# Kernel tuning notes

Measured on AMD Instinct MI355X. Metric: run time of the kernel, lower is better.

Reference implementation:

```python
import jax, jax.numpy as jnp
import numpy as np

N, E, L, F, HID, OUT = 20000, 200000, 5, 4, 128, 3


def _lin(x, w, b):
    # torch Linear convention: w is [out, in]
    return x @ w.T + b


def setup_inputs() -> dict:
    key = jax.random.key(0)
    ks = iter(jax.random.split(key, 40))
    nrm = lambda shape, s=0.05: jax.random.normal(next(ks), shape, dtype=jnp.float32) * s
    inp = {
        'x': jax.random.normal(next(ks), (N, L, F), dtype=jnp.float32),
        'edge_index': jax.random.randint(next(ks), (2, E), 0, N, dtype=jnp.int64),
        'edge_attr': jax.random.normal(next(ks), (E, F), dtype=jnp.float32),
        'batch': jnp.zeros((N,), dtype=jnp.int64),
        'node_type': jax.random.normal(next(ks), (N, 1), dtype=jnp.float32),
        # PastStateEncoder params
        'emb': nrm((L, F), 1.0),
        'conv_w': nrm((HID, 2 * F, 3)),  # Conv1d(8,128,3) OIW
        'conv_b': nrm((HID,)),
        # FusionLayer Linear(129,128)
        'fuse_w': nrm((HID, HID + 1)), 'fuse_b': nrm((HID,)),
        # gnn1 EdgeModel: Linear(2*128+4,128), Linear(128,128)
        'g1e_w1': nrm((HID, 2 * HID + F)), 'g1e_b1': nrm((HID,)),
        'g1e_w2': nrm((HID, HID)), 'g1e_b2': nrm((HID,)),
        # gnn1 NodeModel: Linear(256,128), Linear(128,128)
        'g1n_w1': nrm((HID, 2 * HID)), 'g1n_b1': nrm((HID,)),
        'g1n_w2': nrm((HID, HID)), 'g1n_b2': nrm((HID,)),
        # gnn2 EdgeModel: Linear(2*128+128,128), Linear(128,128)
        'g2e_w1': nrm((HID, 3 * HID)), 'g2e_b1': nrm((HID,)),
        'g2e_w2': nrm((HID, HID)), 'g2e_b2': nrm((HID,)),
        # gnn2 NodeModel
        'g2n_w1': nrm((HID, 2 * HID)), 'g2n_b1': nrm((HID,)),
        'g2n_w2': nrm((HID, HID)), 'g2n_b2': nrm((HID,)),
        # final_mlp: Linear(128,128), BN(128), Linear(128,3)
        'fm_w1': nrm((HID, HID)), 'fm_b1': nrm((HID,)),
        'bn_g': jnp.ones((HID,), dtype=jnp.float32), 'bn_b': jnp.zeros((HID,), dtype=jnp.float32),
        'fm_w2': nrm((OUT, HID)), 'fm_b2': nrm((OUT,)),
    }
    return inp


def _encoder(x, emb, conv_w, conv_b):
    # x: [N, L, F]; append learned positional embedding -> [N, L, 2F]
    n = x.shape[0]
    xe = jnp.concatenate([x, jnp.broadcast_to(emb[None], (n, L, F))], axis=-1)
    xc = xe.transpose(0, 2, 1)  # [N, 2F, L]
    y = jax.lax.conv_general_dilated(
        xc, conv_w, window_strides=(1,), padding=[(1, 1)],
        dimension_numbers=('NCW', 'OIW', 'NCW'))
    y = y + conv_b[None, :, None]
    return y.mean(axis=-1)  # [N, HID]


def _edge_mlp(src, dst, ea, w1, b1, w2, b2):
    h = jax.nn.relu(_lin(jnp.concatenate([src, dst, ea], axis=1), w1, b1))
    return _lin(h, w2, b2)


def _node_mlp(x_row, ea, w1, b1, w2, b2):
    h = jax.nn.relu(_lin(jnp.concatenate([x_row, ea], axis=1), w1, b1))
    return _lin(h, w2, b2)


def reference(x, edge_index, edge_attr, batch, node_type,
              emb, conv_w, conv_b, fuse_w, fuse_b,
              g1e_w1, g1e_b1, g1e_w2, g1e_b2, g1n_w1, g1n_b1, g1n_w2, g1n_b2,
              g2e_w1, g2e_b1, g2e_w2, g2e_b2, g2n_w1, g2n_b1, g2n_w2, g2n_b2,
              fm_w1, fm_b1, bn_g, bn_b, fm_w2, fm_b2):
    row, col = edge_index[0], edge_index[1]
    h = _encoder(x, emb, conv_w, conv_b)                     # [N,128]
    h = _lin(jnp.concatenate([h, node_type], axis=-1), fuse_w, fuse_b)  # [N,128]
    # gnn1 (MetaLayer: edge model then node model; node model here is per-edge)
    ea = _edge_mlp(h[row], h[col], edge_attr, g1e_w1, g1e_b1, g1e_w2, g1e_b2)  # [E,128]
    h = _node_mlp(h[row], ea, g1n_w1, g1n_b1, g1n_w2, g1n_b2)                  # [E,128]
    # gnn2 (h now lives on edges; indices < N <= E remain valid, matching torch)
    ea = _edge_mlp(h[row], h[col], ea, g2e_w1, g2e_b1, g2e_w2, g2e_b2)
    h = _node_mlp(h[row], ea, g2n_w1, g2n_b1, g2n_w2, g2n_b2)
    # final head on edge_attr: Linear -> BatchNorm1d (training stats) -> ReLU -> Linear
    z = _lin(ea, fm_w1, fm_b1)
    mu = z.mean(axis=0)
    var = z.var(axis=0)  # biased, matches torch BN normalization
    z = (z - mu) * jax.lax.rsqrt(var + 1e-5) * bn_g + bn_b
    z = jax.nn.relu(z)
    return _lin(z, fm_w2, fm_b2)  # [E,3]
```

## Files before the change

kernel.cpp:

```cpp
#include <hip/hip_runtime.h>

#define N_NODES 20000
#define N_EDGES 200000
#define HID 128
#define STR 136
#define NBLK 3125

typedef unsigned short u16;
using bf16x8 = __attribute__((ext_vector_type(8))) __bf16;
using f32x4  = __attribute__((ext_vector_type(4))) float;

__device__ __forceinline__ u16 f2bf(float f) {
  union { float f; unsigned u; } v; v.f = f;
  unsigned u = v.u;
  return (u16)((u + 0x7FFFu + ((u >> 16) & 1u)) >> 16);
}
__device__ __forceinline__ float bf2f(unsigned s) {
  union { unsigned u; float f; } v; v.u = s << 16;
  return v.f;
}
__device__ __forceinline__ bf16x8 ld8(const u16* p) { return *(const bf16x8*)p; }

__device__ __forceinline__ void zero_acc(f32x4 acc[4][2]) {
#pragma unroll
  for (int i = 0; i < 4; ++i) {
    acc[i][0] = (f32x4){0.f, 0.f, 0.f, 0.f};
    acc[i][1] = (f32x4){0.f, 0.f, 0.f, 0.f};
  }
}

template <int KSTEPS, typename AF>
__device__ __forceinline__ void wgemm(const u16* __restrict__ PW, AF afrag,
                                      f32x4 acc[4][2], int lane, int wave) {
  const u16* pb = PW + (wave * 2 * 64 + lane) * 8;
  bf16x8 b0[2], b1[2];
  b0[0] = ld8(pb);
  b1[0] = ld8(pb + 512);
#pragma unroll
  for (int ks = 0; ks < KSTEPS; ++ks) {
    const int cur = ks & 1, nxt = cur ^ 1;
    if (ks + 1 < KSTEPS) {
      b0[nxt] = ld8(pb + (ks + 1) * 4096);
      b1[nxt] = ld8(pb + (ks + 1) * 4096 + 512);
    }
#pragma unroll
    for (int mt = 0; mt < 4; ++mt) {
      bf16x8 a = afrag(ks, mt);
      acc[mt][0] = __builtin_amdgcn_mfma_f32_16x16x32_bf16(a, b0[cur], acc[mt][0], 0, 0, 0);
      acc[mt][1] = __builtin_amdgcn_mfma_f32_16x16x32_bf16(a, b1[cur], acc[mt][1], 0, 0, 0);
    }
  }
}

template <bool RELU>
__device__ __forceinline__ void epi_store(u16* buf, const f32x4 acc[4][2],
                                          const float* __restrict__ bias,
                                          int lane, int wave) {
  const int c = lane & 15, q = lane >> 4;
  const float bb0 = bias[wave * 32 + c], bb1 = bias[wave * 32 + 16 + c];
#pragma unroll
  for (int mt = 0; mt < 4; ++mt)
#pragma unroll
    for (int nt = 0; nt < 2; ++nt) {
      const float bb = nt ? bb1 : bb0;
      const int col = wave * 32 + nt * 16 + c;
#pragma unroll
      for (int r = 0; r < 4; ++r) {
        float v = acc[mt][nt][r] + bb;
        if (RELU) v = fmaxf(v, 0.f);
        buf[(mt * 16 + q * 4 + r) * STR + col] = f2bf(v);
      }
    }
}

__device__ __forceinline__ void flush_buf(const u16* buf, u16* __restrict__ gout,
                                          int e0, int tid) {
#pragma unroll
  for (int it = 0; it < 4; ++it) {
    int cid = tid + it * 256, e = cid >> 4, p = cid & 15;
    uint4 v = *(const uint4*)(buf + e * STR + p * 8);
    *(uint4*)(gout + (size_t)(e0 + e) * HID + p * 8) = v;
  }
}

__device__ __forceinline__ void stage_gather(const int* __restrict__ rowI,
                                             const int* __restrict__ colI,
                                             const u16* __restrict__ htab,
                                             u16* B0, u16* B1,
                                             int e0, int lane, int wave) {
  const int r = lane >> 4, p = lane & 15;
#pragma unroll
  for (int it = 0; it < 8; ++it) {
    int j = wave * 32 + it * 4 + r;
    int e = j & 63;
    int id = (j < 64) ? rowI[e0 + e] : colI[e0 + e];
    uint4 v = *(const uint4*)(htab + (size_t)id * HID + p * 8);
    *(uint4*)(((j < 64) ? B0 : B1) + e * STR + p * 8) = v;
  }
}

__global__ void k_fold(const float* __restrict__ emb, const float* __restrict__ conv_w,
                       const float* __restrict__ conv_b, const float* __restrict__ fuse_w,
                       const float* __restrict__ fuse_b,
                       const float* __restrict__ fm_w1, const float* __restrict__ g2e_b2,
                       const float* __restrict__ fm_b1,
                       float* __restrict__ Mt, float* __restrict__ C0,
                       float* __restrict__ Wnt, float* __restrict__ b67) {
  __shared__ float Ash[128][21];
  int o = threadIdx.x;
  {
    float b0 = conv_b[o];
#pragma unroll
    for (int p = 0; p < 5; ++p) {
#pragma unroll
      for (int i = 0; i < 8; ++i) {
        float s = 0.f;
#pragma unroll
        for (int k = 0; k < 3; ++k) {
          int t = p + 1 - k;
          if (t >= 0 && t < 5) s += conv_w[(o * 8 + i) * 3 + k];
        }
        s *= 0.2f;
        if (i < 4) Ash[o][p * 4 + i] = s;
        else b0 += emb[p * 4 + (i - 4)] * s;
      }
    }
    Ash[o][20] = b0;
  }
  __syncthreads();
  float m[20];
#pragma unroll
  for (int qq = 0; qq < 20; ++qq) m[qq] = 0.f;
  float c0 = fuse_b[o];
  for (int j = 0; j < 128; ++j) {
    float w = fuse_w[o * 129 + j];
#pragma unroll
    for (int qq = 0; qq < 20; ++qq) m[qq] += w * Ash[j][qq];
    c0 += w * Ash[j][20];
  }
#pragma unroll
  for (int qq = 0; qq < 20; ++qq) Mt[qq * 128 + o] = m[qq];
  C0[o] = c0;
  Wnt[o] = fuse_w[o * 129 + 128];
  float sb = 0.f;
  for (int j = 0; j < 128; ++j) sb += fm_w1[o * 128 + j] * g2e_b2[j];
  b67[o] = sb + fm_b1[o];
}

__global__ void k_fold2(const float* __restrict__ w6, const float* __restrict__ w7,
                        float* __restrict__ W67) {
  int o = blockIdx.x;
  int k = threadIdx.x;
  float s = 0.f;
  for (int j = 0; j < 128; ++j) s += w7[o * 128 + j] * w6[j * 128 + k];
  W67[o * 128 + k] = s;
}

struct PackArgs {
  const float* src[6];
  u16* dst[6];
  int Kin[6];
  int ksCum[7];
};

__global__ void k_pack(PackArgs pa) {
  int bk = blockIdx.x;
  int mi = 0;
  while (bk >= pa.ksCum[mi + 1]) ++mi;
  int ks = bk - pa.ksCum[mi];
  const float* W = pa.src[mi];
  u16* D = pa.dst[mi] + ks * 4096;
  int Kin = pa.Kin[mi];
#pragma unroll
  for (int t = 0; t < 16; ++t) {
    int el = t * 256 + (int)threadIdx.x;
    int j = el & 7, ln = (el >> 3) & 63, ntile = el >> 9;
    int k = ks * 32 + ((ln >> 4) << 3) + j;
    int n = ntile * 16 + (ln & 15);
    float v = (k < Kin) ? W[n * Kin + k] : 0.0f;
    D[el] = f2bf(v);
  }
}

__global__ __launch_bounds__(256) void k_encode(const float* __restrict__ x,
                                                const float* __restrict__ node_type,
                                                const float* __restrict__ Mt,
                                                const float* __restrict__ C0,
                                                const float* __restrict__ Wnt,
                                                u16* __restrict__ h2) {
  __shared__ float xs[16][20], nts[16], mts[20 * 128];
  const int tid = threadIdx.x;
  const int n0 = blockIdx.x * 16;
  for (int i = tid; i < 320; i += 256) xs[i / 20][i % 20] = x[n0 * 20 + i];
  if (tid < 16) nts[tid] = node_type[n0 + tid];
  for (int i = tid; i < 2560; i += 256) mts[i] = Mt[i];
  __syncthreads();
  const int nl = tid >> 4;
  const int c0 = (tid & 15) * 8;
  float nt = nts[nl];
  union { u16 s[8]; uint4 u; } o;
#pragma unroll
  for (int i = 0; i < 8; ++i) {
    int ch = c0 + i;
    float acc = C0[ch] + Wnt[ch] * nt;
#pragma unroll
    for (int qq = 0; qq < 20; ++qq) acc += xs[nl][qq] * mts[qq * 128 + ch];
    o.s[i] = f2bf(acc);
  }
  *(uint4*)(h2 + (size_t)(n0 + nl) * HID + c0) = o.u;
}

__global__ __launch_bounds__(256, 4) void k_gnn1(
    const int* __restrict__ eidx, const float* __restrict__ eattr,
    const u16* __restrict__ h2, const u16* __restrict__ pW1, const u16* __restrict__ pW2,
    const u16* __restrict__ pW3, const u16* __restrict__ pW4, const float* __restrict__ b1,
    const float* __restrict__ b2, const float* __restrict__ b3, const float* __restrict__ b4,
    u16* __restrict__ ea1, u16* __restrict__ h3) {
  __shared__ __align__(16) u16 B0[64 * STR], B1[64 * STR];
  const int tid = threadIdx.x, lane = tid & 63, wave = tid >> 6;
  const int e0 = blockIdx.x * 64;
  const int m = lane & 15, q = lane >> 4;
  const int aoff = m * STR + q * 8;
  const int* rowI = eidx;
  const int* colI = eidx + N_EDGES;

  stage_gather(rowI, colI, h2, B0, B1, e0, lane, wave);

  bf16x8 ef[4];
#pragma unroll
  for (int mt = 0; mt < 4; ++mt) {
    union { u16 s[8]; uint4 u; bf16x8 v; } t;
    t.u = make_uint4(0u, 0u, 0u, 0u);
    if (q == 0) {
      float4 a = *(const float4*)(eattr + (size_t)(e0 + mt * 16 + m) * 4);
      t.s[0] = f2bf(a.x); t.s[1] = f2bf(a.y); t.s[2] = f2bf(a.z); t.s[3] = f2bf(a.w);
    }
    ef[mt] = t.v;
  }
  __syncthreads();

  f32x4 acc[4][2];
  zero_acc(acc);
  wgemm<9>(pW1, [&](int ks, int mt) -> bf16x8 {
    if (ks < 4) return ld8(B0 + aoff + mt * 16 * STR + ks * 32);
    if (ks < 8) return ld8(B1 + aoff + mt * 16 * STR + (ks - 4) * 32);
    return ef[mt];
  }, acc, lane, wave);
  __syncthreads();
  epi_store<true>(B1, acc, b1, lane, wave);
  __syncthreads();

  zero_acc(acc);
  wgemm<4>(pW2, [&](int ks, int mt) -> bf16x8 {
    return ld8(B1 + aoff + mt * 16 * STR + ks * 32);
  }, acc, lane, wave);
  epi_store<false>(B0, acc, b2, lane, wave);
  __syncthreads();
  flush_buf(B0, ea1, e0, tid);

  if (e0 < N_NODES) {
#pragma unroll
    for (int it = 0; it < 4; ++it) {
      int e = wave * 16 + it * 4 + q;
      int id = rowI[e0 + e];
      uint4 v = *(const uint4*)(h2 + (size_t)id * HID + m * 8);
      *(uint4*)(B1 + e * STR + m * 8) = v;
    }
    __syncthreads();

    zero_acc(acc);
    wgemm<8>(pW3, [&](int ks, int mt) -> bf16x8 {
      if (ks < 4) return ld8(B1 + aoff + mt * 16 * STR + ks * 32);
      return ld8(B0 + aoff + mt * 16 * STR + (ks - 4) * 32);
    }, acc, lane, wave);
    __syncthreads();
    epi_store<true>(B1, acc, b3, lane, wave);
    __syncthreads();

    zero_acc(acc);
    wgemm<4>(pW4, [&](int ks, int mt) -> bf16x8 {
      return ld8(B1 + aoff + mt * 16 * STR + ks * 32);
    }, acc, lane, wave);
    epi_store<false>(B0, acc, b4, lane, wave);
    __syncthreads();
    flush_buf(B0, h3, e0, tid);
  }
}

__global__ __launch_bounds__(256, 4) void k_gnn2(
    const int* __restrict__ eidx, const u16* __restrict__ h3, u16* ea1z,
    const u16* __restrict__ pW5, const u16* __restrict__ pW67,
    const float* __restrict__ b5, const float* __restrict__ b67,
    float* __restrict__ partials) {
  __shared__ __align__(16) u16 B0[64 * STR], B1[64 * STR];
  const int tid = threadIdx.x, lane = tid & 63, wave = tid >> 6;
  const int e0 = blockIdx.x * 64;
  const int m = lane & 15, q = lane >> 4;
  const int aoff = m * STR + q * 8;
  const int* rowI = eidx;
  const int* colI = eidx + N_EDGES;

  stage_gather(rowI, colI, h3, B0, B1, e0, lane, wave);
  __syncthreads();

  f32x4 acc[4][2];
  zero_acc(acc);
  wgemm<8>(pW5, [&](int ks, int mt) -> bf16x8 {
    if (ks < 4) return ld8(B0 + aoff + mt * 16 * STR + ks * 32);
    return ld8(B1 + aoff + mt * 16 * STR + (ks - 4) * 32);
  }, acc, lane, wave);
  __syncthreads();

#pragma unroll
  for (int it = 0; it < 4; ++it) {
    int cid = tid + it * 256, e = cid >> 4, p = cid & 15;
    uint4 v = *(const uint4*)(ea1z + (size_t)(e0 + e) * HID + p * 8);
    *(uint4*)(B0 + e * STR + p * 8) = v;
  }
  __syncthreads();

  wgemm<4>(pW5 + 8 * 4096, [&](int ks, int mt) -> bf16x8 {
    return ld8(B0 + aoff + mt * 16 * STR + ks * 32);
  }, acc, lane, wave);
  epi_store<true>(B1, acc, b5, lane, wave);
  __syncthreads();

  zero_acc(acc);
  wgemm<4>(pW67, [&](int ks, int mt) -> bf16x8 {
    return ld8(B1 + aoff + mt * 16 * STR + ks * 32);
  }, acc, lane, wave);

  {
    const int c = lane & 15;
    const float bb0 = b67[wave * 32 + c], bb1 = b67[wave * 32 + 16 + c];
    float s0 = 0.f, q0 = 0.f, s1 = 0.f, q1 = 0.f;
#pragma unroll
    for (int mt = 0; mt < 4; ++mt)
#pragma unroll
      for (int r = 0; r < 4; ++r) {
        float v0 = acc[mt][0][r] + bb0;
        float v1 = acc[mt][1][r] + bb1;
        s0 += v0; q0 += v0 * v0;
        s1 += v1; q1 += v1 * v1;
        int row = mt * 16 + q * 4 + r;
        B0[row * STR + wave * 32 + c] = f2bf(v0);
        B0[row * STR + wave * 32 + 16 + c] = f2bf(v1);
      }
    s0 += __shfl_xor(s0, 16); s0 += __shfl_xor(s0, 32);
    q0 += __shfl_xor(q0, 16); q0 += __shfl_xor(q0, 32);
    s1 += __shfl_xor(s1, 16); s1 += __shfl_xor(s1, 32);
    q1 += __shfl_xor(q1, 16); q1 += __shfl_xor(q1, 32);
    if (lane < 16) {
      int base = (int)blockIdx.x * 256;
      partials[base + wave * 32 + lane] = s0;
      partials[base + wave * 32 + 16 + lane] = s1;
      partials[base + 128 + wave * 32 + lane] = q0;
      partials[base + 128 + wave * 32 + 16 + lane] = q1;
    }
  }
  __syncthreads();
  flush_buf(B0, ea1z, e0, tid);
}

__global__ void k_reduce(const float* __restrict__ partials, float* __restrict__ bnacc,
                         int nrows) {
  int t = threadIdx.x;
  float s = 0.f;
  for (int b = blockIdx.x; b < nrows; b += 64) s += partials[b * 256 + t];
  atomicAdd(&bnacc[t], s);
}

__global__ __launch_bounds__(256) void k_head(const u16* __restrict__ z,
                                              const float* __restrict__ bnacc,
                                              const float* __restrict__ bn_g,
                                              const float* __restrict__ bn_b,
                                              const float* __restrict__ w2,
                                              const float* __restrict__ b2,
                                              float* __restrict__ out) {
  __shared__ float sh_s[128], sh_h[128], sh_w0[128], sh_w1[128], sh_w2[128];
  const int tid = threadIdx.x;
  if (tid < 128) {
    const float inv = 1.0f / (float)N_EDGES;
    float mu = bnacc[tid] * inv;
    float var = bnacc[128 + tid] * inv - mu * mu;
    float sc = bn_g[tid] * rsqrtf(var + 1e-5f);
    sh_s[tid] = sc;
    sh_h[tid] = bn_b[tid] - mu * sc;
    sh_w0[tid] = w2[tid];
    sh_w1[tid] = w2[128 + tid];
    sh_w2[tid] = w2[256 + tid];
  }
  __syncthreads();
  const int e = blockIdx.x * 256 + tid;
  if (e >= N_EDGES) return;
  float a0 = b2[0], a1 = b2[1], a2 = b2[2];
  const u16* zr = z + (size_t)e * HID;
#pragma unroll
  for (int p = 0; p < 16; ++p) {
    uint4 v = *(const uint4*)(zr + p * 8);
    unsigned wv[4] = {v.x, v.y, v.z, v.w};
#pragma unroll
    for (int k = 0; k < 4; ++k) {
      int ch = p * 8 + k * 2;
      float lo = bf2f(wv[k] & 0xffffu), hi = bf2f(wv[k] >> 16);
      float r0 = fmaxf(fmaf(lo, sh_s[ch], sh_h[ch]), 0.f);
      float r1 = fmaxf(fmaf(hi, sh_s[ch + 1], sh_h[ch + 1]), 0.f);
      a0 += r0 * sh_w0[ch] + r1 * sh_w0[ch + 1];
      a1 += r0 * sh_w1[ch] + r1 * sh_w1[ch + 1];
      a2 += r0 * sh_w2[ch] + r1 * sh_w2[ch + 1];
    }
  }
  out[e * 3 + 0] = a0;
  out[e * 3 + 1] = a1;
  out[e * 3 + 2] = a2;
}

extern "C" void kernel_launch(void* const* d_in, const int* in_sizes, int n_in,
                              void* d_out, int out_size, void* d_ws, size_t ws_size,
                              hipStream_t stream) {
  const float* x         = (const float*)d_in[0];
  const int* eidx        = (const int*)d_in[1];
  const float* eattr     = (const float*)d_in[2];
  const float* node_type = (const float*)d_in[4];
  const float* emb       = (const float*)d_in[5];
  const float* conv_w    = (const float*)d_in[6];
  const float* conv_b    = (const float*)d_in[7];
  const float* fuse_w    = (const float*)d_in[8];
  const float* fuse_b    = (const float*)d_in[9];
  const float* g1e_w1    = (const float*)d_in[10];
  const float* g1e_b1    = (const float*)d_in[11];
  const float* g1e_w2    = (const float*)d_in[12];
  const float* g1e_b2    = (const float*)d_in[13];
  const float* g1n_w1    = (const float*)d_in[14];
  const float* g1n_b1    = (const float*)d_in[15];
  const float* g1n_w2    = (const float*)d_in[16];
  const float* g1n_b2    = (const float*)d_in[17];
  const float* g2e_w1    = (const float*)d_in[18];
  const float* g2e_b1    = (const float*)d_in[19];
  const float* g2e_w2    = (const float*)d_in[20];
  const float* g2e_b2    = (const float*)d_in[21];
  const float* fm_w1     = (const float*)d_in[26];
  const float* fm_b1     = (const float*)d_in[27];
  const float* bn_g      = (const float*)d_in[28];
  const float* bn_b      = (const float*)d_in[29];
  const float* fm_w2     = (const float*)d_in[30];
  const float* fm_b2     = (const float*)d_in[31];
  float* out = (float*)d_out;

  char* ws = (char*)d_ws;
  size_t off = 0;
  auto take = [&](size_t bytes) {
    void* p = ws + off;
    off = (off + bytes + 255) & ~(size_t)255;
    return p;
  };
  u16* h2   = (u16*)take((size_t)N_NODES * HID * 2);
  u16* h3   = (u16*)take((size_t)20032 * HID * 2);
  u16* ea1z = (u16*)take((size_t)N_EDGES * HID * 2);
  float* Mt    = (float*)take(20 * 128 * 4);
  float* C0    = (float*)take(128 * 4);
  float* Wnt   = (float*)take(128 * 4);
  float* bnacc = (float*)take(256 * 4);
  float* b67   = (float*)take(128 * 4);
  float* W67f  = (float*)take(128 * 128 * 4);
  float* partials = (float*)take((size_t)NBLK * 256 * 4);
  u16* pW1  = (u16*)take(9 * 4096 * 2);
  u16* pW2  = (u16*)take(4 * 4096 * 2);
  u16* pW3  = (u16*)take(8 * 4096 * 2);
  u16* pW4  = (u16*)take(4 * 4096 * 2);
  u16* pW5  = (u16*)take(12 * 4096 * 2);
  u16* pW67 = (u16*)take(4 * 4096 * 2);

  hipMemsetAsync(bnacc, 0, 256 * 4, stream);
  k_fold<<<1, 128, 0, stream>>>(emb, conv_w, conv_b, fuse_w, fuse_b,
                                fm_w1, g2e_b2, fm_b1, Mt, C0, Wnt, b67);
  k_fold2<<<128, 128, 0, stream>>>(g2e_w2, fm_w1, W67f);

  PackArgs pa;
  const float* srcs[6] = {g1e_w1, g1e_w2, g1n_w1, g1n_w2, g2e_w1, W67f};
  u16* dsts[6] = {pW1, pW2, pW3, pW4, pW5, pW67};
  int kins[6] = {260, 128, 256, 128, 384, 128};
  int kst[6] = {9, 4, 8, 4, 12, 4};
  int cum = 0;
  for (int i = 0; i < 6; ++i) {
    pa.src[i] = srcs[i]; pa.dst[i] = dsts[i]; pa.Kin[i] = kins[i];
    pa.ksCum[i] = cum; cum += kst[i];
  }
  pa.ksCum[6] = cum;
  k_pack<<<41, 256, 0, stream>>>(pa);

  k_encode<<<N_NODES / 16, 256, 0, stream>>>(x, node_type, Mt, C0, Wnt, h2);
  k_gnn1<<<NBLK, 256, 0, stream>>>(eidx, eattr, h2, pW1, pW2, pW3, pW4,
                                   g1e_b1, g1e_b2, g1n_b1, g1n_b2, ea1z, h3);
  k_gnn2<<<NBLK, 256, 0, stream>>>(eidx, h3, ea1z, pW5, pW67,
                                   g2e_b1, b67, partials);
  k_reduce<<<64, 256, 0, stream>>>(partials, bnacc, NBLK);
  k_head<<<(N_EDGES + 255) / 256, 256, 0, stream>>>(ea1z, bnacc, bn_g, bn_b,
                                                    fm_w2, fm_b2, out);
}
```

Before: 277.3 us.

## Merge prep kernels, use replicated atomic BN stats, and coalesce head reads

Folds k_fold and k_fold2 into one 128-block prep kernel that parallelises the weight folding across blocks, and merges weight packing with node encoding into a single launch. The per-block BN partials buffer and the k_reduce kernel are replaced by atomics into 64 replicated slots, which k_head sums itself. k_head now has each group of 16 lanes read one edge row contiguously and reduce with shuffles, so global loads coalesce. This cuts launch count and memory traffic, at the cost of atomic contention and nondeterministic float summation order.

Measured after the change: 237.5 us. 1.17x faster.

```diff
diff --git a/kernel.cpp b/kernel.cpp
--- a/kernel.cpp
+++ b/kernel.cpp
@@ -5,6 +5,7 @@
 #define HID 128
 #define STR 136
 #define NBLK 3125
+#define NREP 64
 
 typedef unsigned short u16;
 using bf16x8 = __attribute__((ext_vector_type(8))) __bf16;
@@ -99,17 +100,21 @@
   }
 }
 
-__global__ void k_fold(const float* __restrict__ emb, const float* __restrict__ conv_w,
-                       const float* __restrict__ conv_b, const float* __restrict__ fuse_w,
-                       const float* __restrict__ fuse_b,
-                       const float* __restrict__ fm_w1, const float* __restrict__ g2e_b2,
-                       const float* __restrict__ fm_b1,
-                       float* __restrict__ Mt, float* __restrict__ C0,
-                       float* __restrict__ Wnt, float* __restrict__ b67) {
-  __shared__ float Ash[128][21];
-  int o = threadIdx.x;
+__global__ __launch_bounds__(128) void k_prep1(
+    const float* __restrict__ emb, const float* __restrict__ conv_w,
+    const float* __restrict__ conv_b, const float* __restrict__ fuse_w,
+    const float* __restrict__ fuse_b,
+    const float* __restrict__ fm_w1, const float* __restrict__ g2e_b2,
+    const float* __restrict__ fm_b1, const float* __restrict__ w6,
+    float* __restrict__ Mt, float* __restrict__ C0, float* __restrict__ Wnt,
+    float* __restrict__ b67, float* __restrict__ W67) {
+  __shared__ float red[22][129];
+  __shared__ float w7s[128];
+  const int o = blockIdx.x;
+  const int j = threadIdx.x;
+  float A[21];
   {
-    float b0 = conv_b[o];
+    float b0 = conv_b[j];
 #pragma unroll
     for (int p = 0; p < 5; ++p) {
 #pragma unroll
@@ -118,42 +123,33 @@
 #pragma unroll
         for (int k = 0; k < 3; ++k) {
           int t = p + 1 - k;
-          if (t >= 0 && t < 5) s += conv_w[(o * 8 + i) * 3 + k];
+          if (t >= 0 && t < 5) s += conv_w[(j * 8 + i) * 3 + k];
         }
         s *= 0.2f;
-        if (i < 4) Ash[o][p * 4 + i] = s;
+        if (i < 4) A[p * 4 + i] = s;
         else b0 += emb[p * 4 + (i - 4)] * s;
       }
     }
-    Ash[o][20] = b0;
-  }
-  __syncthreads();
-  float m[20];
-#pragma unroll
-  for (int qq = 0; qq < 20; ++qq) m[qq] = 0.f;
-  float c0 = fuse_b[o];
-  for (int j = 0; j < 128; ++j) {
-    float w = fuse_w[o * 129 + j];
-#pragma unroll
-    for (int qq = 0; qq < 20; ++qq) m[qq] += w * Ash[j][qq];
-    c0 += w * Ash[j][20];
-  }
-#pragma unroll
-  for (int qq = 0; qq < 20; ++qq) Mt[qq * 128 + o] = m[qq];
-  C0[o] = c0;
-  Wnt[o] = fuse_w[o * 129 + 128];
-  float sb = 0.f;
-  for (int j = 0; j < 128; ++j) sb += fm_w1[o * 128 + j] * g2e_b2[j];
-  b67[o] = sb + fm_b1[o];
-}
-
-__global__ void k_fold2(const float* __restrict__ w6, const float* __restrict__ w7,
-                        float* __restrict__ W67) {
-  int o = blockIdx.x;
-  int k = threadIdx.x;
+    A[20] = b0;
+  }
+  float w = fuse_w[o * 129 + j];
+  float w7 = fm_w1[o * 128 + j];
+  w7s[j] = w7;
+#pragma unroll
+  for (int qq = 0; qq < 21; ++qq) red[qq][j] = w * A[qq];
+  red[21][j] = w7 * g2e_b2[j];
+  __syncthreads();
+  if (j < 22) {
+    float s = 0.f;
+    for (int t = 0; t < 128; ++t) s += red[j][t];
+    if (j < 20)      Mt[j * 128 + o] = s;
+    else if (j == 20) C0[o] = s + fuse_b[o];
+    else              b67[o] = s + fm_b1[o];
+  }
+  if (j == 0) Wnt[o] = fuse_w[o * 129 + 128];
   float s = 0.f;
-  for (int j = 0; j < 128; ++j) s += w7[o * 128 + j] * w6[j * 128 + k];
-  W67[o * 128 + k] = s;
+  for (int t = 0; t < 128; ++t) s += w7s[t] * w6[t * 128 + j];
+  W67[o * 128 + j] = s;
 }
 
 struct PackArgs {
@@ -163,34 +159,32 @@
   int ksCum[7];
 };
 
-__global__ void k_pack(PackArgs pa) {
-  int bk = blockIdx.x;
-  int mi = 0;
-  while (bk >= pa.ksCum[mi + 1]) ++mi;
-  int ks = bk - pa.ksCum[mi];
-  const float* W = pa.src[mi];
-  u16* D = pa.dst[mi] + ks * 4096;
-  int Kin = pa.Kin[mi];
-#pragma unroll
-  for (int t = 0; t < 16; ++t) {
-    int el = t * 256 + (int)threadIdx.x;
-    int j = el & 7, ln = (el >> 3) & 63, ntile = el >> 9;
-    int k = ks * 32 + ((ln >> 4) << 3) + j;
-    int n = ntile * 16 + (ln & 15);
-    float v = (k < Kin) ? W[n * Kin + k] : 0.0f;
-    D[el] = f2bf(v);
-  }
-}
-
-__global__ __launch_bounds__(256) void k_encode(const float* __restrict__ x,
-                                                const float* __restrict__ node_type,
-                                                const float* __restrict__ Mt,
-                                                const float* __restrict__ C0,
-                                                const float* __restrict__ Wnt,
-                                                u16* __restrict__ h2) {
+__global__ __launch_bounds__(256) void k_prep2(
+    PackArgs pa, const float* __restrict__ x, const float* __restrict__ node_type,
+    const float* __restrict__ Mt, const float* __restrict__ C0,
+    const float* __restrict__ Wnt, u16* __restrict__ h2) {
+  if (blockIdx.x < 41) {
+    int bk = blockIdx.x;
+    int mi = 0;
+    while (bk >= pa.ksCum[mi + 1]) ++mi;
+    int ks = bk - pa.ksCum[mi];
+    const float* W = pa.src[mi];
+    u16* D = pa.dst[mi] + ks * 4096;
+    int Kin = pa.Kin[mi];
+#pragma unroll
+    for (int t = 0; t < 16; ++t) {
+      int el = t * 256 + (int)threadIdx.x;
+      int j = el & 7, ln = (el >> 3) & 63, ntile = el >> 9;
+      int k = ks * 32 + ((ln >> 4) << 3) + j;
+      int n = ntile * 16 + (ln & 15);
+      float v = (k < Kin) ? W[n * Kin + k] : 0.0f;
+      D[el] = f2bf(v);
+    }
+    return;
+  }
   __shared__ float xs[16][20], nts[16], mts[20 * 128];
   const int tid = threadIdx.x;
-  const int n0 = blockIdx.x * 16;
+  const int n0 = ((int)blockIdx.x - 41) * 16;
   for (int i = tid; i < 320; i += 256) xs[i / 20][i % 20] = x[n0 * 20 + i];
   if (tid < 16) nts[tid] = node_type[n0 + tid];
   for (int i = tid; i < 2560; i += 256) mts[i] = Mt[i];
@@ -291,7 +285,7 @@
     const int* __restrict__ eidx, const u16* __restrict__ h3, u16* ea1z,
     const u16* __restrict__ pW5, const u16* __restrict__ pW67,
     const float* __restrict__ b5, const float* __restrict__ b67,
-    float* __restrict__ partials) {
+    float* __restrict__ bnrep) {
   __shared__ __align__(16) u16 B0[64 * STR], B1[64 * STR];
   const int tid = threadIdx.x, lane = tid & 63, wave = tid >> 6;
   const int e0 = blockIdx.x * 64;
@@ -351,27 +345,19 @@
     s1 += __shfl_xor(s1, 16); s1 += __shfl_xor(s1, 32);
     q1 += __shfl_xor(q1, 16); q1 += __shfl_xor(q1, 32);
     if (lane < 16) {
-      int base = (int)blockIdx.x * 256;
-      partials[base + wave * 32 + lane] = s0;
-      partials[base + wave * 32 + 16 + lane] = s1;
-      partials[base + 128 + wave * 32 + lane] = q0;
-      partials[base + 128 + wave * 32 + 16 + lane] = q1;
+      float* slot = bnrep + ((int)blockIdx.x & (NREP - 1)) * 256;
+      atomicAdd(&slot[wave * 32 + lane], s0);
+      atomicAdd(&slot[wave * 32 + 16 + lane], s1);
+      atomicAdd(&slot[128 + wave * 32 + lane], q0);
+      atomicAdd(&slot[128 + wave * 32 + 16 + lane], q1);
     }
   }
   __syncthreads();
   flush_buf(B0, ea1z, e0, tid);
 }
 
-__global__ void k_reduce(const float* __restrict__ partials, float* __restrict__ bnacc,
-                         int nrows) {
-  int t = threadIdx.x;
-  float s = 0.f;
-  for (int b = blockIdx.x; b < nrows; b += 64) s += partials[b * 256 + t];
-  atomicAdd(&bnacc[t], s);
-}
-
 __global__ __launch_bounds__(256) void k_head(const u16* __restrict__ z,
-                                              const float* __restrict__ bnacc,
+                                              const float* __restrict__ bnrep,
                                               const float* __restrict__ bn_g,
                                               const float* __restrict__ bn_b,
                                               const float* __restrict__ w2,
@@ -379,29 +365,40 @@
                                               float* __restrict__ out) {
   __shared__ float sh_s[128], sh_h[128], sh_w0[128], sh_w1[128], sh_w2[128];
   const int tid = threadIdx.x;
-  if (tid < 128) {
-    const float inv = 1.0f / (float)N_EDGES;
-    float mu = bnacc[tid] * inv;
-    float var = bnacc[128 + tid] * inv - mu * mu;
-    float sc = bn_g[tid] * rsqrtf(var + 1e-5f);
-    sh_s[tid] = sc;
-    sh_h[tid] = bn_b[tid] - mu * sc;
-    sh_w0[tid] = w2[tid];
-    sh_w1[tid] = w2[128 + tid];
-    sh_w2[tid] = w2[256 + tid];
-  }
-  __syncthreads();
-  const int e = blockIdx.x * 256 + tid;
-  if (e >= N_EDGES) return;
-  float a0 = b2[0], a1 = b2[1], a2 = b2[2];
-  const u16* zr = z + (size_t)e * HID;
-#pragma unroll
-  for (int p = 0; p < 16; ++p) {
-    uint4 v = *(const uint4*)(zr + p * 8);
+  {
+    float s = 0.f;
+    for (int r = 0; r < NREP; ++r) s += bnrep[r * 256 + tid];
+    __shared__ float acc2[256];
+    acc2[tid] = s;
+    __syncthreads();
+    if (tid < 128) {
+      const float inv = 1.0f / (float)N_EDGES;
+      float mu = acc2[tid] * inv;
+      float var = acc2[128 + tid] * inv - mu * mu;
+      float sc = bn_g[tid] * rsqrtf(var + 1e-5f);
+      sh_s[tid] = sc;
+      sh_h[tid] = bn_b[tid] - mu * sc;
+      sh_w0[tid] = w2[tid];
+      sh_w1[tid] = w2[128 + tid];
+      sh_w2[tid] = w2[256 + tid];
+    }
+    __syncthreads();
+  }
+  const int lane = tid & 63, wave = tid >> 6;
+  const int g = lane >> 4;
+  const int p = lane & 15;
+  const int c0 = p * 8;
+  const float bb0 = b2[0], bb1 = b2[1], bb2 = b2[2];
+#pragma unroll 4
+  for (int it = 0; it < 16; ++it) {
+    int e = (int)blockIdx.x * 256 + wave * 64 + it * 4 + g;
+    if (e >= N_EDGES) break;
+    uint4 v = *(const uint4*)(z + (size_t)e * HID + c0);
     unsigned wv[4] = {v.x, v.y, v.z, v.w};
+    float a0 = 0.f, a1 = 0.f, a2 = 0.f;
 #pragma unroll
     for (int k = 0; k < 4; ++k) {
-      int ch = p * 8 + k * 2;
+      int ch = c0 + k * 2;
       float lo = bf2f(wv[k] & 0xffffu), hi = bf2f(wv[k] >> 16);
       float r0 = fmaxf(fmaf(lo, sh_s[ch], sh_h[ch]), 0.f);
       float r1 = fmaxf(fmaf(hi, sh_s[ch + 1], sh_h[ch + 1]), 0.f);
@@ -409,10 +406,14 @@
       a1 += r0 * sh_w1[ch] + r1 * sh_w1[ch + 1];
       a2 += r0 * sh_w2[ch] + r1 * sh_w2[ch + 1];
     }
-  }
-  out[e * 3 + 0] = a0;
-  out[e * 3 + 1] = a1;
-  out[e * 3 + 2] = a2;
+#pragma unroll
+    for (int off = 1; off < 16; off <<= 1) {
+      a0 += __shfl_xor(a0, off);
+      a1 += __shfl_xor(a1, off);
+      a2 += __shfl_xor(a2, off);
+    }
+    if (p < 3) out[e * 3 + p] = (p == 0) ? a0 + bb0 : (p == 1) ? a1 + bb1 : a2 + bb2;
+  }
 }
 
 extern "C" void kernel_launch(void* const* d_in, const int* in_sizes, int n_in,
@@ -460,10 +461,9 @@
   float* Mt    = (float*)take(20 * 128 * 4);
   float* C0    = (float*)take(128 * 4);
   float* Wnt   = (float*)take(128 * 4);
-  float* bnacc = (float*)take(256 * 4);
   float* b67   = (float*)take(128 * 4);
   float* W67f  = (float*)take(128 * 128 * 4);
-  float* partials = (float*)take((size_t)NBLK * 256 * 4);
+  float* bnrep = (float*)take((size_t)NREP * 256 * 4);
   u16* pW1  = (u16*)take(9 * 4096 * 2);
   u16* pW2  = (u16*)take(4 * 4096 * 2);
   u16* pW3  = (u16*)take(8 * 4096 * 2);
@@ -471,10 +471,10 @@
   u16* pW5  = (u16*)take(12 * 4096 * 2);
   u16* pW67 = (u16*)take(4 * 4096 * 2);
 
-  hipMemsetAsync(bnacc, 0, 256 * 4, stream);
-  k_fold<<<1, 128, 0, stream>>>(emb, conv_w, conv_b, fuse_w, fuse_b,
-                                fm_w1, g2e_b2, fm_b1, Mt, C0, Wnt, b67);
-  k_fold2<<<128, 128, 0, stream>>>(g2e_w2, fm_w1, W67f);
+  hipMemsetAsync(bnrep, 0, (size_t)NREP * 256 * 4, stream);
+  k_prep1<<<128, 128, 0, stream>>>(emb, conv_w, conv_b, fuse_w, fuse_b,
+                                   fm_w1, g2e_b2, fm_b1, g2e_w2,
+                                   Mt, C0, Wnt, b67, W67f);
 
   PackArgs pa;
   const float* srcs[6] = {g1e_w1, g1e_w2, g1n_w1, g1n_w2, g2e_w1, W67f};
@@ -487,14 +487,12 @@
     pa.ksCum[i] = cum; cum += kst[i];
   }
   pa.ksCum[6] = cum;
-  k_pack<<<41, 256, 0, stream>>>(pa);
-
-  k_encode<<<N_NODES / 16, 256, 0, stream>>>(x, node_type, Mt, C0, Wnt, h2);
+
+  k_prep2<<<41 + N_NODES / 16, 256, 0, stream>>>(pa, x, node_type, Mt, C0, Wnt, h2);
   k_gnn1<<<NBLK, 256, 0, stream>>>(eidx, eattr, h2, pW1, pW2, pW3, pW4,
                                    g1e_b1, g1e_b2, g1n_b1, g1n_b2, ea1z, h3);
   k_gnn2<<<NBLK, 256, 0, stream>>>(eidx, h3, ea1z, pW5, pW67,
-                                   g2e_b1, b67, partials);
-  k_reduce<<<64, 256, 0, stream>>>(partials, bnacc, NBLK);
-  k_head<<<(N_EDGES + 255) / 256, 256, 0, stream>>>(ea1z, bnacc, bn_g, bn_b,
+                                   g2e_b1, b67, bnrep);
+  k_head<<<(N_EDGES + 255) / 256, 256, 0, stream>>>(ea1z, bnrep, bn_g, bn_b,
                                                     fm_w2, fm_b2, out);
 }
```
